# Kernel optimization log

Measured on AMD Instinct MI355X. Metric: run time of the kernel, lower is better.

The kernel has to match this reference:

```python
import jax, jax.numpy as jnp
import numpy as np

N = 100000   # nodes
E = 3200000  # edges (avg degree 32)
G = 1024     # graphs in batch
H = 16       # hidden_dim


def setup_inputs() -> dict:
    key = jax.random.key(0)
    ks = jax.random.split(key, 12)
    p = lambda k, s: jax.random.normal(k, s, dtype=jnp.float32) * 0.1
    return {
        "types": jax.random.randint(ks[0], (N,), 0, 3),
        "pos": jax.random.randint(ks[1], (N,), 0, 3),
        "edge_index": jax.random.randint(ks[2], (2, E), 0, N),
        "batch": jnp.sort(jax.random.randint(ks[3], (N,), 0, G)),
        "W1": p(ks[4], (3, H)), "b1": jnp.zeros((H,), jnp.float32),
        "W2": p(ks[5], (3, H)), "b2": jnp.zeros((H,), jnp.float32),
        "Wg0": p(ks[6], (2 * H, H)), "bg0": jnp.zeros((H,), jnp.float32),
        "Wg1": p(ks[7], (H, H)), "bg1": jnp.zeros((H,), jnp.float32),
        "Wg2": p(ks[8], (H, H)), "bg2": jnp.zeros((H,), jnp.float32),
        "Wo": p(ks[9], (H, 1)), "bo": jnp.zeros((1,), jnp.float32),
    }


def reference(types, pos, edge_index, batch, W1, b1, W2, b2,
              Wg0, bg0, Wg1, bg1, Wg2, bg2, Wo, bo):
    # one-hot encode + linear embed
    xt = jax.nn.one_hot(types, 3, dtype=jnp.float32) @ W1 + b1   # [N, H]
    xp = jax.nn.one_hot(pos, 3, dtype=jnp.float32) @ W2 + b2     # [N, H]
    z = jnp.concatenate([xt, xp], axis=-1)                        # [N, 2H]

    src, dst = edge_index[0], edge_index[1]
    # GCN symmetric normalization with self-loops (gcn_norm)
    deg = jax.ops.segment_sum(jnp.ones((E,), jnp.float32), dst, num_segments=N) + 1.0
    dis = jax.lax.rsqrt(deg)                                      # D^{-1/2}
    edge_coef = (dis[src] * dis[dst])[:, None]                    # [E, 1]
    self_coef = (dis * dis)[:, None]                              # [N, 1]

    def gcn_conv(x, W, b):
        h = x @ W                                                 # [N, H]
        agg = jax.ops.segment_sum(h[src] * edge_coef, dst, num_segments=N)
        return agg + h * self_coef + b

    z = jax.nn.relu(gcn_conv(z, Wg0, bg0))  # dropout=0.2 is train-only; eval mode
    z = jax.nn.relu(gcn_conv(z, Wg1, bg1))
    z = gcn_conv(z, Wg2, bg2)               # no act after last layer

    # global_mean_pool over graph ids
    cnt = jax.ops.segment_sum(jnp.ones((N,), jnp.float32), batch, num_segments=G)
    pooled = jax.ops.segment_sum(z, batch, num_segments=G) / jnp.maximum(cnt, 1.0)[:, None]
    return pooled @ Wo + bo                                       # [G, 1]
```

## Files before the change

### kernel.cpp

```cpp
#include <hip/hip_runtime.h>
#include <hip/hip_fp16.h>

#define NN 100000
#define NE 3200000
#define NG 1024
#define NP 100352
#define NBUCK 391
#define NBLK 256
#define CHUNK ((NE + NBLK - 1) / NBLK)
#define WINCAP 12288
#define BATCH 32

static __device__ inline void acc_u2(float4& acc, uint2 u) {
    __half2* ph = reinterpret_cast<__half2*>(&u);
    float2 lo = __half22float2(ph[0]);
    float2 hi = __half22float2(ph[1]);
    acc.x += lo.x; acc.y += lo.y; acc.z += hi.x; acc.w += hi.y;
}
static __device__ inline uint2 pack4(float a, float b, float c, float d) {
    __half2 lo = __floats2half2_rn(a, b);
    __half2 hi = __floats2half2_rn(c, d);
    uint2 u;
    u.x = *reinterpret_cast<unsigned int*>(&lo);
    u.y = *reinterpret_cast<unsigned int*>(&hi);
    return u;
}
static __device__ inline float4 shfl_xor4(float4 v, int m) {
    float4 r;
    r.x = __shfl_xor(v.x, m); r.y = __shfl_xor(v.y, m);
    r.z = __shfl_xor(v.z, m); r.w = __shfl_xor(v.w, m);
    return r;
}

__global__ void hist_buckets(const int* __restrict__ dst, int* __restrict__ bcnt) {
    __shared__ int sm[NBUCK];
    int tid = threadIdx.x;
    for (int i = tid; i < NBUCK; i += 256) sm[i] = 0;
    __syncthreads();
    int s = blockIdx.x * CHUNK, e = min(NE, s + CHUNK);
    for (int i = s + tid; i < e; i += 256)
        atomicAdd(&sm[__builtin_nontemporal_load(&dst[i]) >> 8], 1);
    __syncthreads();
    for (int i = tid; i < NBUCK; i += 256)
        if (sm[i]) atomicAdd(&bcnt[i], sm[i]);
}

__global__ void scan_buckets(const int* __restrict__ bcnt, int* __restrict__ bbase) {
    __shared__ int tmp[512];
    int tid = threadIdx.x;
    int v = (tid < NBUCK) ? bcnt[tid] : 0;
    tmp[tid] = v;
    __syncthreads();
    for (int off = 1; off < 512; off <<= 1) {
        int t = (tid >= off) ? tmp[tid - off] : 0;
        __syncthreads();
        tmp[tid] += t;
        __syncthreads();
    }
    if (tid < NBUCK) bbase[tid] = tmp[tid] - v;
}

__global__ void partition(const int* __restrict__ src, const int* __restrict__ dst,
                          const int* __restrict__ bbase, int* __restrict__ bfill,
                          int* __restrict__ part) {
    __shared__ int smh[NBUCK];
    __shared__ int smc[NBUCK];
    int tid = threadIdx.x;
    for (int i = tid; i < NBUCK; i += 256) smh[i] = 0;
    __syncthreads();
    int s = blockIdx.x * CHUNK, e = min(NE, s + CHUNK);
    for (int i = s + tid; i < e; i += 256)
        atomicAdd(&smh[__builtin_nontemporal_load(&dst[i]) >> 8], 1);
    __syncthreads();
    for (int i = tid; i < NBUCK; i += 256) {
        int c = smh[i];
        smc[i] = c ? (bbase[i] + atomicAdd(&bfill[i], c)) : 0;
    }
    __syncthreads();
    for (int i = s + tid; i < e; i += 256) {
        int d = __builtin_nontemporal_load(&dst[i]);
        int sv = __builtin_nontemporal_load(&src[i]);
        int b = d >> 8;
        int p = atomicAdd(&smc[b], 1);
        part[p] = sv | ((d & 255) << 17);
    }
}

__global__ void build_csr(const int* __restrict__ part, const int* __restrict__ bbase,
                          const int* __restrict__ bcnt, int* __restrict__ cnt,
                          int* __restrict__ offs, float* __restrict__ dis,
                          int* __restrict__ srcs) {
    __shared__ int sm_cnt[256];
    __shared__ int sm_off[256];
    __shared__ int sm_cur[256];
    __shared__ int sm_win[WINCAP];
    int b = blockIdx.x, tid = threadIdx.x;
    int base = bbase[b], m = bcnt[b];
    sm_cnt[tid] = 0;
    __syncthreads();
    for (int i = tid; i < m; i += 256)
        atomicAdd(&sm_cnt[__builtin_nontemporal_load(&part[base + i]) >> 17], 1);
    __syncthreads();
    int v = sm_cnt[tid];
    sm_off[tid] = v;
    __syncthreads();
    for (int off = 1; off < 256; off <<= 1) {
        int t = (tid >= off) ? sm_off[tid - off] : 0;
        __syncthreads();
        sm_off[tid] += t;
        __syncthreads();
    }
    int excl = sm_off[tid] - v;
    int n = b * 256 + tid;
    if (n < NN) {
        cnt[n] = v;
        offs[n] = base + excl;
        dis[n] = rsqrtf((float)v + 1.0f);
    }
    sm_cur[tid] = excl;
    __syncthreads();
    if (m <= WINCAP) {
        for (int i = tid; i < m; i += 256) {
            int p = __builtin_nontemporal_load(&part[base + i]);
            int l = atomicAdd(&sm_cur[p >> 17], 1);
            sm_win[l] = p & 0x1FFFF;
        }
        __syncthreads();
        for (int i = tid; i < m; i += 256) srcs[base + i] = sm_win[i];
    } else {
        for (int i = tid; i < m; i += 256) {
            int p = __builtin_nontemporal_load(&part[base + i]);
            int l = atomicAdd(&sm_cur[p >> 17], 1);
            srcs[base + l] = p & 0x1FFFF;
        }
    }
}

__global__ void embed_tf0(const int* __restrict__ types, const int* __restrict__ pos,
                          const float* __restrict__ W1, const float* __restrict__ b1,
                          const float* __restrict__ W2, const float* __restrict__ b2,
                          const float* __restrict__ Wg0, const float* __restrict__ dis,
                          uint2* __restrict__ hs) {
    __shared__ float sW[32 * 16];
    int tid = threadIdx.x;
    sW[tid] = Wg0[tid];
    sW[tid + 256] = Wg0[tid + 256];
    __syncthreads();
    int n = blockIdx.x * 256 + tid;
    if (n >= NN) return;
    int ty = types[n], pp = pos[n];
    float z[32];
#pragma unroll
    for (int j = 0; j < 16; j++) z[j] = W1[ty * 16 + j] + b1[j];
#pragma unroll
    for (int j = 0; j < 16; j++) z[16 + j] = W2[pp * 16 + j] + b2[j];
    float dn = dis[n];
    uint2 o[4];
#pragma unroll
    for (int q = 0; q < 4; q++) {
        float hv[4];
#pragma unroll
        for (int m = 0; m < 4; m++) {
            float a = 0.0f;
#pragma unroll
            for (int k = 0; k < 32; k++) a += z[k] * sW[k * 16 + q * 4 + m];
            hv[m] = a * dn;
        }
        o[q] = pack4(hv[0], hv[1], hv[2], hv[3]);
    }
#pragma unroll
    for (int q = 0; q < 4; q++) hs[(size_t)n * 4 + q] = o[q];
}

template <int RELU, int FUSE_POOL>
__global__ __launch_bounds__(256, 2)
void agg_tf(const uint2* __restrict__ hs, const int* __restrict__ srcs,
            const int* __restrict__ offs, const int* __restrict__ cnt,
            const float* __restrict__ dis, const float* __restrict__ bias,
            const float* __restrict__ Wn, uint2* __restrict__ hs_out,
            const int* __restrict__ batch,
            float* __restrict__ pool, int* __restrict__ gcnt) {
    __shared__ float sW[256];
    int tid = threadIdx.x;
    if (!FUSE_POOL) {
        sW[tid] = Wn[tid];
        __syncthreads();
    }
    int gid = blockIdx.x * 256 + tid;
    int n = gid >> 3;
    int q = gid & 3;
    int c = (gid >> 2) & 1;
    if (n >= NN) return;
    int beg = offs[n], deg = cnt[n];
    float dn = dis[n];
    int half = deg >> 1;
    int i0 = c ? half : 0;
    int iend = c ? deg : half;
    float4 acc = make_float4(0.f, 0.f, 0.f, 0.f);
    for (int i = i0; i < iend; i += BATCH) {
        uint2 a[BATCH];
#pragma unroll
        for (int j = 0; j < BATCH; j++) {
            int idx = i + j;
            int s = __builtin_nontemporal_load(&srcs[beg + idx]);
            s = (idx < iend) ? s : NN;
            a[j] = hs[(size_t)s * 4 + q];
        }
#pragma unroll
        for (int j = 0; j < BATCH; j++) acc_u2(acc, a[j]);
    }
    acc.x += __shfl_xor(acc.x, 4);
    acc.y += __shfl_xor(acc.y, 4);
    acc.z += __shfl_xor(acc.z, 4);
    acc.w += __shfl_xor(acc.w, 4);
    if (c != 0) return;
    acc_u2(acc, hs[(size_t)n * 4 + q]);
    float4 b4 = ((const float4*)bias)[q];
    acc.x = fmaf(acc.x, dn, b4.x);
    acc.y = fmaf(acc.y, dn, b4.y);
    acc.z = fmaf(acc.z, dn, b4.z);
    acc.w = fmaf(acc.w, dn, b4.w);
    if (RELU) {
        acc.x = fmaxf(acc.x, 0.f); acc.y = fmaxf(acc.y, 0.f);
        acc.z = fmaxf(acc.z, 0.f); acc.w = fmaxf(acc.w, 0.f);
    }
    if (FUSE_POOL) {
        float4 w4 = ((const float4*)Wn)[q];
        float s = acc.x * w4.x + acc.y * w4.y + acc.z * w4.z + acc.w * w4.w;
        s += __shfl_xor(s, 1);
        s += __shfl_xor(s, 2);
        if (q == 0) {
            int g = batch[n];
            atomicAdd(&pool[g], s);
            atomicAdd(&gcnt[g], 1);
        }
    } else {
        float4 vals[4];
        vals[0] = acc;
        vals[1] = shfl_xor4(acc, 1);
        vals[2] = shfl_xor4(acc, 2);
        vals[3] = shfl_xor4(acc, 3);
        const float4* sW4 = (const float4*)sW;
        float4 hv = make_float4(0.f, 0.f, 0.f, 0.f);
#pragma unroll
        for (int m = 0; m < 4; m++) {
            float4 v = vals[m];
            int rb = (q ^ m) << 2;
            float4 w;
            w = sW4[(rb + 0) * 4 + q];
            hv.x += v.x * w.x; hv.y += v.x * w.y; hv.z += v.x * w.z; hv.w += v.x * w.w;
            w = sW4[(rb + 1) * 4 + q];
            hv.x += v.y * w.x; hv.y += v.y * w.y; hv.z += v.y * w.z; hv.w += v.y * w.w;
            w = sW4[(rb + 2) * 4 + q];
            hv.x += v.z * w.x; hv.y += v.z * w.y; hv.z += v.z * w.z; hv.w += v.z * w.w;
            w = sW4[(rb + 3) * 4 + q];
            hv.x += v.w * w.x; hv.y += v.w * w.y; hv.z += v.w * w.z; hv.w += v.w * w.w;
        }
        hs_out[(size_t)n * 4 + q] = pack4(hv.x * dn, hv.y * dn, hv.z * dn, hv.w * dn);
    }
}

__global__ void finalize(const float* __restrict__ pool, const int* __restrict__ gcnt,
                         const float* __restrict__ bo, float* __restrict__ out) {
    int g = blockIdx.x * 256 + threadIdx.x;
    if (g < NG) {
        float c = fmaxf((float)gcnt[g], 1.0f);
        out[g] = pool[g] / c + bo[0];
    }
}

extern "C" void kernel_launch(void* const* d_in, const int* in_sizes, int n_in,
                              void* d_out, int out_size, void* d_ws, size_t ws_size,
                              hipStream_t stream) {
    const int*   types = (const int*)d_in[0];
    const int*   pos   = (const int*)d_in[1];
    const int*   ei    = (const int*)d_in[2];
    const int*   batch = (const int*)d_in[3];
    const float* W1  = (const float*)d_in[4];
    const float* b1  = (const float*)d_in[5];
    const float* W2  = (const float*)d_in[6];
    const float* b2  = (const float*)d_in[7];
    const float* Wg0 = (const float*)d_in[8];
    const float* bg0 = (const float*)d_in[9];
    const float* Wg1 = (const float*)d_in[10];
    const float* bg1 = (const float*)d_in[11];
    const float* Wg2 = (const float*)d_in[12];
    const float* bg2 = (const float*)d_in[13];
    const float* Wo  = (const float*)d_in[14];
    const float* bo  = (const float*)d_in[15];
    float* out = (float*)d_out;

    const int* esrc = ei;
    const int* edst = ei + NE;

    int*   bcnt  = (int*)d_ws;
    int*   bfill = bcnt + 512;
    float* pool  = (float*)(bfill + 512);
    int*   gcnt  = (int*)(pool + NG);
    int*   bbase = gcnt + NG;
    int*   cnt   = bbase + 512;
    int*   offs  = cnt + NP;
    float* dis   = (float*)(offs + NP);
    int*   srcs  = (int*)(dis + NP);
    int*   part  = srcs + NE;
    uint2* hsA   = (uint2*)part;
    uint2* hsB   = (uint2*)(part + NE / 2);
    (void)ws_size; (void)n_in; (void)in_sizes; (void)out_size;

    hipMemsetAsync(d_ws, 0, (size_t)(1024 + 2 * NG) * sizeof(int), stream);

    const int NB256 = (NN + 255) / 256;
    const int QB8 = (NN * 8 + 255) / 256;

    hist_buckets<<<NBLK, 256, 0, stream>>>(edst, bcnt);
    scan_buckets<<<1, 512, 0, stream>>>(bcnt, bbase);
    partition<<<NBLK, 256, 0, stream>>>(esrc, edst, bbase, bfill, part);
    build_csr<<<NBUCK, 256, 0, stream>>>(part, bbase, bcnt, cnt, offs, dis, srcs);

    hipMemsetAsync((char*)hsA + (size_t)NN * 32, 0, (size_t)(NP - NN) * 32, stream);
    hipMemsetAsync((char*)hsB + (size_t)NN * 32, 0, (size_t)(NP - NN) * 32, stream);

    embed_tf0<<<NB256, 256, 0, stream>>>(types, pos, W1, b1, W2, b2, Wg0, dis, hsA);
    agg_tf<1, 0><<<QB8, 256, 0, stream>>>(hsA, srcs, offs, cnt, dis, bg0, Wg1, hsB,
                                          batch, pool, gcnt);
    agg_tf<1, 0><<<QB8, 256, 0, stream>>>(hsB, srcs, offs, cnt, dis, bg1, Wg2, hsA,
                                          batch, pool, gcnt);
    agg_tf<0, 1><<<QB8, 256, 0, stream>>>(hsA, srcs, offs, cnt, dis, bg2, Wo, hsB ,
                                          batch, pool, gcnt);

    finalize<<<(NG + 255) / 256, 256, 0, stream>>>(pool, gcnt, bo, out);
}
```

Before: 365.0 us.

## Gather 16-byte half8 rows with 4 threads per node in GCN aggregation

```diff
diff --git a/kernel.cpp b/kernel.cpp
--- a/kernel.cpp
+++ b/kernel.cpp
@@ -9,27 +9,28 @@
 #define NBLK 256
 #define CHUNK ((NE + NBLK - 1) / NBLK)
 #define WINCAP 12288
-#define BATCH 32
-
-static __device__ inline void acc_u2(float4& acc, uint2 u) {
-    __half2* ph = reinterpret_cast<__half2*>(&u);
-    float2 lo = __half22float2(ph[0]);
-    float2 hi = __half22float2(ph[1]);
-    acc.x += lo.x; acc.y += lo.y; acc.z += hi.x; acc.w += hi.y;
-}
-static __device__ inline uint2 pack4(float a, float b, float c, float d) {
-    __half2 lo = __floats2half2_rn(a, b);
-    __half2 hi = __floats2half2_rn(c, d);
-    uint2 u;
-    u.x = *reinterpret_cast<unsigned int*>(&lo);
-    u.y = *reinterpret_cast<unsigned int*>(&hi);
+#define BATCH 8
+
+static __device__ inline void acc8_u4(float* acc, uint4 u) {
+    const __half2* ph = reinterpret_cast<const __half2*>(&u);
+#pragma unroll
+    for (int k = 0; k < 4; k++) {
+        float2 f = __half22float2(ph[k]);
+        acc[2 * k + 0] += f.x;
+        acc[2 * k + 1] += f.y;
+    }
+}
+static __device__ inline uint4 pack8(const float* v) {
+    uint4 u;
+    __half2 h0 = __floats2half2_rn(v[0], v[1]);
+    __half2 h1 = __floats2half2_rn(v[2], v[3]);
+    __half2 h2 = __floats2half2_rn(v[4], v[5]);
+    __half2 h3 = __floats2half2_rn(v[6], v[7]);
+    u.x = *reinterpret_cast<unsigned int*>(&h0);
+    u.y = *reinterpret_cast<unsigned int*>(&h1);
+    u.z = *reinterpret_cast<unsigned int*>(&h2);
+    u.w = *reinterpret_cast<unsigned int*>(&h3);
     return u;
-}
-static __device__ inline float4 shfl_xor4(float4 v, int m) {
-    float4 r;
-    r.x = __shfl_xor(v.x, m); r.y = __shfl_xor(v.y, m);
-    r.z = __shfl_xor(v.z, m); r.w = __shfl_xor(v.w, m);
-    return r;
 }
 
 __global__ void hist_buckets(const int* __restrict__ dst, int* __restrict__ bcnt) {
@@ -140,7 +141,7 @@
                           const float* __restrict__ W1, const float* __restrict__ b1,
                           const float* __restrict__ W2, const float* __restrict__ b2,
                           const float* __restrict__ Wg0, const float* __restrict__ dis,
-                          uint2* __restrict__ hs) {
+                          uint4* __restrict__ hs) {
     __shared__ float sW[32 * 16];
     int tid = threadIdx.x;
     sW[tid] = Wg0[tid];
@@ -155,29 +156,24 @@
 #pragma unroll
     for (int j = 0; j < 16; j++) z[16 + j] = W2[pp * 16 + j] + b2[j];
     float dn = dis[n];
-    uint2 o[4];
-#pragma unroll
-    for (int q = 0; q < 4; q++) {
-        float hv[4];
-#pragma unroll
-        for (int m = 0; m < 4; m++) {
-            float a = 0.0f;
-#pragma unroll
-            for (int k = 0; k < 32; k++) a += z[k] * sW[k * 16 + q * 4 + m];
-            hv[m] = a * dn;
-        }
-        o[q] = pack4(hv[0], hv[1], hv[2], hv[3]);
-    }
-#pragma unroll
-    for (int q = 0; q < 4; q++) hs[(size_t)n * 4 + q] = o[q];
+    float hv[16];
+#pragma unroll
+    for (int j = 0; j < 16; j++) {
+        float a = 0.0f;
+#pragma unroll
+        for (int k = 0; k < 32; k++) a += z[k] * sW[k * 16 + j];
+        hv[j] = a * dn;
+    }
+    hs[(size_t)n * 2 + 0] = pack8(hv);
+    hs[(size_t)n * 2 + 1] = pack8(hv + 8);
 }
 
 template <int RELU, int FUSE_POOL>
-__global__ __launch_bounds__(256, 2)
-void agg_tf(const uint2* __restrict__ hs, const int* __restrict__ srcs,
+__global__ __launch_bounds__(256, 4)
+void agg_tf(const uint4* __restrict__ hs, const int* __restrict__ srcs,
             const int* __restrict__ offs, const int* __restrict__ cnt,
             const float* __restrict__ dis, const float* __restrict__ bias,
-            const float* __restrict__ Wn, uint2* __restrict__ hs_out,
+            const float* __restrict__ Wn, uint4* __restrict__ hs_out,
             const int* __restrict__ batch,
             float* __restrict__ pool, int* __restrict__ gcnt) {
     __shared__ float sW[256];
@@ -187,76 +183,72 @@
         __syncthreads();
     }
     int gid = blockIdx.x * 256 + tid;
-    int n = gid >> 3;
-    int q = gid & 3;
-    int c = (gid >> 2) & 1;
+    int n = gid >> 2;
+    int q = gid & 1;
+    int c = (gid >> 1) & 1;
     if (n >= NN) return;
     int beg = offs[n], deg = cnt[n];
     float dn = dis[n];
     int half = deg >> 1;
     int i0 = c ? half : 0;
     int iend = c ? deg : half;
-    float4 acc = make_float4(0.f, 0.f, 0.f, 0.f);
+    float acc[8] = {0.f, 0.f, 0.f, 0.f, 0.f, 0.f, 0.f, 0.f};
     for (int i = i0; i < iend; i += BATCH) {
-        uint2 a[BATCH];
+        uint4 g[BATCH];
 #pragma unroll
         for (int j = 0; j < BATCH; j++) {
             int idx = i + j;
             int s = __builtin_nontemporal_load(&srcs[beg + idx]);
             s = (idx < iend) ? s : NN;
-            a[j] = hs[(size_t)s * 4 + q];
-        }
-#pragma unroll
-        for (int j = 0; j < BATCH; j++) acc_u2(acc, a[j]);
-    }
-    acc.x += __shfl_xor(acc.x, 4);
-    acc.y += __shfl_xor(acc.y, 4);
-    acc.z += __shfl_xor(acc.z, 4);
-    acc.w += __shfl_xor(acc.w, 4);
+            g[j] = hs[(size_t)s * 2 + q];
+        }
+#pragma unroll
+        for (int j = 0; j < BATCH; j++) acc8_u4(acc, g[j]);
+    }
+#pragma unroll
+    for (int k = 0; k < 8; k++) acc[k] += __shfl_xor(acc[k], 2);
     if (c != 0) return;
-    acc_u2(acc, hs[(size_t)n * 4 + q]);
-    float4 b4 = ((const float4*)bias)[q];
-    acc.x = fmaf(acc.x, dn, b4.x);
-    acc.y = fmaf(acc.y, dn, b4.y);
-    acc.z = fmaf(acc.z, dn, b4.z);
-    acc.w = fmaf(acc.w, dn, b4.w);
-    if (RELU) {
-        acc.x = fmaxf(acc.x, 0.f); acc.y = fmaxf(acc.y, 0.f);
-        acc.z = fmaxf(acc.z, 0.f); acc.w = fmaxf(acc.w, 0.f);
+    uint4 self = hs[(size_t)n * 2 + q];
+    acc8_u4(acc, self);
+#pragma unroll
+    for (int k = 0; k < 8; k++) {
+        acc[k] = fmaf(acc[k], dn, bias[q * 8 + k]);
+        if (RELU) acc[k] = fmaxf(acc[k], 0.f);
     }
     if (FUSE_POOL) {
-        float4 w4 = ((const float4*)Wn)[q];
-        float s = acc.x * w4.x + acc.y * w4.y + acc.z * w4.z + acc.w * w4.w;
+        float s = 0.f;
+#pragma unroll
+        for (int k = 0; k < 8; k++) s += acc[k] * Wn[q * 8 + k];
         s += __shfl_xor(s, 1);
-        s += __shfl_xor(s, 2);
         if (q == 0) {
             int g = batch[n];
             atomicAdd(&pool[g], s);
             atomicAdd(&gcnt[g], 1);
         }
     } else {
-        float4 vals[4];
-        vals[0] = acc;
-        vals[1] = shfl_xor4(acc, 1);
-        vals[2] = shfl_xor4(acc, 2);
-        vals[3] = shfl_xor4(acc, 3);
-        const float4* sW4 = (const float4*)sW;
-        float4 hv = make_float4(0.f, 0.f, 0.f, 0.f);
-#pragma unroll
-        for (int m = 0; m < 4; m++) {
-            float4 v = vals[m];
-            int rb = (q ^ m) << 2;
-            float4 w;
-            w = sW4[(rb + 0) * 4 + q];
-            hv.x += v.x * w.x; hv.y += v.x * w.y; hv.z += v.x * w.z; hv.w += v.x * w.w;
-            w = sW4[(rb + 1) * 4 + q];
-            hv.x += v.y * w.x; hv.y += v.y * w.y; hv.z += v.y * w.z; hv.w += v.y * w.w;
-            w = sW4[(rb + 2) * 4 + q];
-            hv.x += v.z * w.x; hv.y += v.z * w.y; hv.z += v.z * w.z; hv.w += v.z * w.w;
-            w = sW4[(rb + 3) * 4 + q];
-            hv.x += v.w * w.x; hv.y += v.w * w.y; hv.z += v.w * w.z; hv.w += v.w * w.w;
-        }
-        hs_out[(size_t)n * 4 + q] = pack4(hv.x * dn, hv.y * dn, hv.z * dn, hv.w * dn);
+        float oth[8];
+#pragma unroll
+        for (int k = 0; k < 8; k++) oth[k] = __shfl_xor(acc[k], 1);
+        float zlo[8], zhi[8];
+#pragma unroll
+        for (int k = 0; k < 8; k++) {
+            zlo[k] = (q == 0) ? acc[k] : oth[k];
+            zhi[k] = (q == 0) ? oth[k] : acc[k];
+        }
+        float hv[8] = {0.f, 0.f, 0.f, 0.f, 0.f, 0.f, 0.f, 0.f};
+#pragma unroll
+        for (int k = 0; k < 8; k++) {
+            const float* wl = &sW[k * 16 + q * 8];
+            const float* wh = &sW[(k + 8) * 16 + q * 8];
+#pragma unroll
+            for (int j = 0; j < 8; j++) {
+                hv[j] += zlo[k] * wl[j];
+                hv[j] += zhi[k] * wh[j];
+            }
+        }
+#pragma unroll
+        for (int j = 0; j < 8; j++) hv[j] *= dn;
+        hs_out[(size_t)n * 2 + q] = pack8(hv);
     }
 }
 
@@ -303,14 +295,14 @@
     float* dis   = (float*)(offs + NP);
     int*   srcs  = (int*)(dis + NP);
     int*   part  = srcs + NE;
-    uint2* hsA   = (uint2*)part;
-    uint2* hsB   = (uint2*)(part + NE / 2);
+    uint4* hsA   = (uint4*)part;
+    uint4* hsB   = (uint4*)(part + NE / 2);
     (void)ws_size; (void)n_in; (void)in_sizes; (void)out_size;
 
     hipMemsetAsync(d_ws, 0, (size_t)(1024 + 2 * NG) * sizeof(int), stream);
 
     const int NB256 = (NN + 255) / 256;
-    const int QB8 = (NN * 8 + 255) / 256;
+    const int QB4 = (NN * 4 + 255) / 256;
 
     hist_buckets<<<NBLK, 256, 0, stream>>>(edst, bcnt);
     scan_buckets<<<1, 512, 0, stream>>>(bcnt, bbase);
@@ -321,11 +313,11 @@
     hipMemsetAsync((char*)hsB + (size_t)NN * 32, 0, (size_t)(NP - NN) * 32, stream);
 
     embed_tf0<<<NB256, 256, 0, stream>>>(types, pos, W1, b1, W2, b2, Wg0, dis, hsA);
-    agg_tf<1, 0><<<QB8, 256, 0, stream>>>(hsA, srcs, offs, cnt, dis, bg0, Wg1, hsB,
+    agg_tf<1, 0><<<QB4, 256, 0, stream>>>(hsA, srcs, offs, cnt, dis, bg0, Wg1, hsB,
                                           batch, pool, gcnt);
-    agg_tf<1, 0><<<QB8, 256, 0, stream>>>(hsB, srcs, offs, cnt, dis, bg1, Wg2, hsA,
+    agg_tf<1, 0><<<QB4, 256, 0, stream>>>(hsB, srcs, offs, cnt, dis, bg1, Wg2, hsA,
                                           batch, pool, gcnt);
-    agg_tf<0, 1><<<QB8, 256, 0, stream>>>(hsA, srcs, offs, cnt, dis, bg2, Wo, hsB ,
+    agg_tf<0, 1><<<QB4, 256, 0, stream>>>(hsA, srcs, offs, cnt, dis, bg2, Wo, hsB ,
                                           batch, pool, gcnt);
 
     finalize<<<(NG + 255) / 256, 256, 0, stream>>>(pool, gcnt, bo, out);
```

Measured after the change: 342.7 us. 1.06x faster.
